# Performance work log

Measured on AMD Instinct MI355X. Metric: run time of the kernel, lower is better.

Reference implementation:

```python
import jax, jax.numpy as jnp
import numpy as np

B, T, HID = 2, 2048, 2048
H, D, QC = 16, 128, 512
RD, THETA = 64, 10000.0
WIN = 512
G, INTER = 4, 2048
EPS = 1e-6


def _rope_cache(t):
    inv = 1.0 / (THETA ** (jnp.arange(0, RD, 2, dtype=jnp.float32) / RD))  # (RD/2,)
    ang = jnp.arange(t, dtype=jnp.float32)[:, None] * inv[None, :]          # (t, RD/2)
    return jnp.cos(ang), jnp.sin(ang)


def _apply_partial_rope(x, cos, sin):
    # x: (..., t, D); rotate first RD channels (rotate-half convention)
    x_rot, x_pass = x[..., :RD], x[..., RD:]
    x1, x2 = x_rot[..., : RD // 2], x_rot[..., RD // 2 :]
    r1 = x1 * cos - x2 * sin
    r2 = x1 * sin + x2 * cos
    return jnp.concatenate([r1, r2, x_pass], axis=-1)


def _rmsnorm(x, w):
    return x * jax.lax.rsqrt(jnp.mean(x * x, axis=-1, keepdims=True) + EPS) * w


def setup_inputs() -> dict:
    key = jax.random.key(0)
    ks = jax.random.split(key, 10)
    s = 0.02
    return {
        "h": jax.random.normal(ks[0], (B, T, HID), jnp.float32),
        "wq_comp": jax.random.normal(ks[1], (HID, QC), jnp.float32) * s,
        "wq_up": jax.random.normal(ks[2], (QC, H * D), jnp.float32) * s,
        "wk": jax.random.normal(ks[3], (HID, D), jnp.float32) * s,
        "wv": jax.random.normal(ks[4], (HID, D), jnp.float32) * s,
        "q_norm_w": jnp.ones((D,), jnp.float32),
        "k_norm_w": jnp.ones((D,), jnp.float32),
        "sink_logit": jnp.zeros((H,), jnp.float32),
        "out_w1": jax.random.normal(ks[5], (G, (H // G) * D, INTER), jnp.float32) * s,
        "out_w2": jax.random.normal(ks[6], (G * INTER, HID), jnp.float32) * s,
    }


def reference(h, wq_comp, wq_up, wk, wv, q_norm_w, k_norm_w, sink_logit, out_w1, out_w2):
    b, t, _ = h.shape
    cos, sin = _rope_cache(t)
    # queries: compress -> up -> (b,H,t,D)
    q = (h @ wq_comp) @ wq_up
    q = q.reshape(b, t, H, D).transpose(0, 2, 1, 3)
    q = _rmsnorm(_apply_partial_rope(q, cos, sin), q_norm_w)
    # single shared K/V head (b,t,D)
    k = _rmsnorm(_apply_partial_rope(h @ wk, cos, sin), k_norm_w)
    v = h @ wv
    i = jnp.arange(t)
    diff = i[:, None] - i[None, :]
    mask = (diff >= 0) & (diff < WIN)  # (t,t)
    # scores (b,H,t,t) + sink column
    scale = 1.0 / jnp.sqrt(jnp.asarray(D, h.dtype))
    scores = jnp.einsum("bhtd,bsd->bhts", q, k) * scale
    scores = jnp.where(mask[None, None], scores, jnp.asarray(-1e30, h.dtype))
    sink = jnp.broadcast_to(sink_logit[None, :, None, None], (b, H, t, 1))
    probs = jax.nn.softmax(jnp.concatenate([scores, sink], axis=-1), axis=-1)
    attn = jnp.einsum("bhts,bsd->bhtd", probs[..., :t], v)  # sink mass dropped
    # grouped output projection
    x = attn.transpose(0, 2, 1, 3).reshape(b, t, G, (H // G) * D)
    x = jnp.einsum("btgi,gio->btgo", x, out_w1).reshape(b, t, G * INTER)
    return x @ out_w2
```

## Files before the change

### kernel.cpp

```cpp
#include <hip/hip_runtime.h>
#include <hip/hip_bf16.h>
#include <stdint.h>

typedef __hip_bfloat16 bf16;
typedef __bf16 bf16x8 __attribute__((ext_vector_type(8)));
typedef float f32x4 __attribute__((ext_vector_type(4)));

#define B_ 2
#define T_ 2048
#define HID_ 2048
#define H_ 16
#define D_ 128
#define WIN_ 512

__device__ __forceinline__ void async_copy16(const void* g, void* l) {
  __builtin_amdgcn_global_load_lds(
      (__attribute__((address_space(1))) void*)(uintptr_t)g,
      (__attribute__((address_space(3))) void*)(uint32_t)(uintptr_t)l,
      16, 0, 0);
}

__device__ __forceinline__ void block_sync() {
  asm volatile("" ::: "memory");
  __builtin_amdgcn_s_barrier();
  asm volatile("" ::: "memory");
}

__global__ __launch_bounds__(256) void cvt4_all(
    const float* __restrict__ h, const float* __restrict__ w1, bf16* __restrict__ outh, bf16* __restrict__ outw1)
{
  int i = blockIdx.x * 256 + threadIdx.x;
  const int NH = 2097152;
  const float* in; bf16* out;
  if (i < NH) { in = h; out = outh; }
  else { i -= NH; in = w1; out = outw1; }
  const float4 v = ((const float4*)in)[i];
  bf16* p = out + (size_t)i * 4;
  p[0] = __float2bfloat16(v.x);
  p[1] = __float2bfloat16(v.y);
  p[2] = __float2bfloat16(v.z);
  p[3] = __float2bfloat16(v.w);
}

__global__ __launch_bounds__(256) void cvtT_all(
    const float* __restrict__ wqc, const float* __restrict__ wk, const float* __restrict__ wv,
    const float* __restrict__ wqu, bf16* __restrict__ qkvT, bf16* __restrict__ wquT)
{
  __shared__ bf16 tile[32][33];
  const int id = blockIdx.x;
  const float* in; bf16* out; int R, C, bx, by;
  if (id < 1024)      { int l = id;        in = wqc; out = qkvT;                      R = 2048; C = 512;  bx = (l & 15) * 32; by = (l >> 4) * 32; }
  else if (id < 1280) { int l = id - 1024; in = wk;  out = qkvT + (size_t)512 * 2048; R = 2048; C = 128;  bx = (l & 3) * 32;  by = (l >> 2) * 32; }
  else if (id < 1536) { int l = id - 1280; in = wv;  out = qkvT + (size_t)640 * 2048; R = 2048; C = 128;  bx = (l & 3) * 32;  by = (l >> 2) * 32; }
  else                { int l = id - 1536; in = wqu; out = wquT;                      R = 512;  C = 2048; bx = (l & 63) * 32; by = (l >> 6) * 32; }
  const int tx = threadIdx.x & 31, ty = threadIdx.x >> 5;
#pragma unroll
  for (int i = 0; i < 32; i += 8)
    tile[ty+i][tx] = __float2bfloat16(in[(size_t)(by + ty + i)*C + bx + tx]);
  __syncthreads();
#pragma unroll
  for (int i = 0; i < 32; i += 8)
    out[(size_t)(bx + ty + i)*R + by + tx] = tile[tx][ty+i];
}

__global__ __launch_bounds__(256) void cvtT(
    const float* __restrict__ in, bf16* __restrict__ out, int R, int C)
{
  __shared__ bf16 tile[32][33];
  const int bx = blockIdx.x*32, by = blockIdx.y*32;
  const int tx = threadIdx.x & 31, ty = threadIdx.x >> 5;
#pragma unroll
  for (int i = 0; i < 32; i += 8)
    tile[ty+i][tx] = __float2bfloat16(in[(size_t)(by + ty + i)*C + bx + tx]);
  __syncthreads();
#pragma unroll
  for (int i = 0; i < 32; i += 8)
    out[(size_t)(bx + ty + i)*R + by + tx] = tile[tx][ty+i];
}

__global__ __launch_bounds__(256) void transpose_k(
    const bf16* __restrict__ in, bf16* __restrict__ out,
    int R, int C, int ldin, int ldout, long long inBatch, long long outBatch)
{
  __shared__ bf16 tile[32][33];
  in  += (size_t)blockIdx.z * inBatch;
  out += (size_t)blockIdx.z * outBatch;
  const int bx = blockIdx.x*32, by = blockIdx.y*32;
  const int tx = threadIdx.x & 31, ty = threadIdx.x >> 5;
#pragma unroll
  for (int i = 0; i < 32; i += 8)
    tile[ty+i][tx] = in[(size_t)(by + ty + i)*ldin + bx + tx];
  __syncthreads();
#pragma unroll
  for (int i = 0; i < 32; i += 8)
    out[(size_t)(bx + ty + i)*ldout + by + tx] = tile[tx][ty+i];
}

template <bool F32OUT>
__global__ __launch_bounds__(256) void gemm_bt(
    const bf16* __restrict__ Ab, const bf16* __restrict__ Bb, void* __restrict__ Cb,
    int K, int lda, int ldb, int ldc,
    long long sAz, long long sBz, long long sCz)
{
  const bf16* A = Ab + (size_t)blockIdx.z * sAz;
  const bf16* B = Bb + (size_t)blockIdx.z * sBz;
  __shared__ __align__(16) __bf16 sa[128*64];
  __shared__ __align__(16) __bf16 sb[128*64];
  const int bm = blockIdx.x * 128, bn = blockIdx.y * 128;
  const int t = threadIdx.x;
  const int wave = t >> 6, lane = t & 63;
  const int fm = lane & 15, quad = lane >> 4;
  const int wm = (wave & 1) * 64, wn = (wave >> 1) * 64;
  const int arow0 = t >> 3;
  const int acol_sw = (((t & 7) ^ (arow0 & 7)) << 3);
  const int fsw = fm & 7;

  f32x4 acc[4][4];
#pragma unroll
  for (int i = 0; i < 4; ++i)
#pragma unroll
    for (int j = 0; j < 4; ++j) acc[i][j] = {0.f, 0.f, 0.f, 0.f};

  for (int k0 = 0; k0 < K; k0 += 64) {
    __syncthreads();
#pragma unroll
    for (int i = 0; i < 4; ++i)
      async_copy16(&A[(size_t)(bm + arow0 + i*32)*lda + k0 + acol_sw], &sa[(size_t)(i*256 + wave*64)*8]);
#pragma unroll
    for (int i = 0; i < 4; ++i)
      async_copy16(&B[(size_t)(bn + arow0 + i*32)*ldb + k0 + acol_sw], &sb[(size_t)(i*256 + wave*64)*8]);
    __syncthreads();
#pragma unroll
    for (int ks = 0; ks < 64; ks += 32) {
      bf16x8 av[4], bv[4];
#pragma unroll
      for (int mt = 0; mt < 4; ++mt)
        av[mt] = *(const bf16x8*)&sa[(wm + mt*16 + fm)*64 + ((((ks>>3) + quad) ^ fsw) << 3)];
#pragma unroll
      for (int nt = 0; nt < 4; ++nt)
        bv[nt] = *(const bf16x8*)&sb[(wn + nt*16 + fm)*64 + ((((ks>>3) + quad) ^ fsw) << 3)];
#pragma unroll
      for (int mt = 0; mt < 4; ++mt)
#pragma unroll
        for (int nt = 0; nt < 4; ++nt)
          acc[mt][nt] = __builtin_amdgcn_mfma_f32_16x16x32_bf16(av[mt], bv[nt], acc[mt][nt], 0, 0, 0);
    }
  }
  if constexpr (F32OUT) {
    float* C = (float*)Cb + (size_t)blockIdx.z * sCz;
#pragma unroll
    for (int mt = 0; mt < 4; ++mt)
#pragma unroll
      for (int r = 0; r < 4; ++r) {
        const int row = bm + wm + mt*16 + quad*4 + r;
#pragma unroll
        for (int nt = 0; nt < 4; ++nt)
          C[(size_t)row*ldc + bn + wn + nt*16 + fm] = acc[mt][nt][r];
      }
  } else {
    bf16* C = (bf16*)Cb + (size_t)blockIdx.z * sCz;
#pragma unroll
    for (int mt = 0; mt < 4; ++mt)
#pragma unroll
      for (int r = 0; r < 4; ++r) {
        const int row = bm + wm + mt*16 + quad*4 + r;
#pragma unroll
        for (int nt = 0; nt < 4; ++nt)
          C[(size_t)row*ldc + bn + wn + nt*16 + fm] = __float2bfloat16(acc[mt][nt][r]);
      }
  }
}

template <bool F32OUT>
__global__ __launch_bounds__(512, 2) void gemm_bt8(
    const bf16* __restrict__ Ab, const bf16* __restrict__ Bb, void* __restrict__ Cb,
    int K, int lda, int ldb, int ldc,
    long long sAz, long long sBz, long long sCz)
{
  const bf16* A = Ab + (size_t)blockIdx.z * sAz;
  const bf16* B = Bb + (size_t)blockIdx.z * sBz;
  __shared__ __align__(16) __bf16 sA[2][256*64];
  __shared__ __align__(16) __bf16 sB[2][128*64];
  const int bm = blockIdx.x * 256, bn = blockIdx.y * 128;
  const int t = threadIdx.x;
  const int wave = t >> 6, lane = t & 63;
  const int fm = lane & 15, quad = lane >> 4, fsw = fm & 7;
  const int wave_m = wave >> 1, wave_n = wave & 1;
  const int srow = t >> 3;
  const int cchunk = (t & 7) ^ (srow & 7);
  const int NT = K >> 6;

  auto stage = [&](int tile, int o) {
    if (tile >= NT) return;
    const int par = tile & 1;
    const int kc = (tile << 6) + (cchunk << 3);
    if (o < 2) {
      async_copy16(&B[(size_t)(bn + (o << 6) + srow)*ldb + kc],
                   &sB[par][(size_t)((o << 6) + wave*8) * 64]);
    } else {
      const int h = (o - 2) << 7;
      async_copy16(&A[(size_t)(bm + h + srow)*lda + kc],
                   &sA[par][(size_t)(h + wave*8) * 64]);
      async_copy16(&A[(size_t)(bm + h + 64 + srow)*lda + kc],
                   &sA[par][(size_t)(h + 64 + wave*8) * 64]);
    }
  };

  f32x4 acc[4][4];
#pragma unroll
  for (int i = 0; i < 4; ++i)
#pragma unroll
    for (int j = 0; j < 4; ++j) acc[i][j] = {0.f, 0.f, 0.f, 0.f};

  stage(0, 0); stage(0, 1); stage(0, 2); stage(0, 3);
  stage(1, 0); stage(1, 1);
  asm volatile("s_waitcnt vmcnt(2)" ::: "memory");
  block_sync();

  for (int d = 0; d < NT; ++d) {
    const int par = d & 1;
    bf16x8 bfr[4][2];
#pragma unroll
    for (int q = 0; q < 4; ++q) {
      const int arow = wave_m*64 + q*16 + fm;
      const bf16x8 a0 = *(const bf16x8*)&sA[par][(size_t)arow*64 + ((quad ^ fsw) << 3)];
      const bf16x8 a1 = *(const bf16x8*)&sA[par][(size_t)arow*64 + (((4 + quad) ^ fsw) << 3)];
      if (q == 0) {
#pragma unroll
        for (int n = 0; n < 4; ++n) {
          const int brow = wave_n*64 + n*16 + fm;
          bfr[n][0] = *(const bf16x8*)&sB[par][(size_t)brow*64 + ((quad ^ fsw) << 3)];
          bfr[n][1] = *(const bf16x8*)&sB[par][(size_t)brow*64 + (((4 + quad) ^ fsw) << 3)];
        }
      }
      if (q == 0)      stage(d + 1, 2);
      else if (q == 1) stage(d + 1, 3);
      else if (q == 2) stage(d + 2, 0);
      else             stage(d + 2, 1);
      block_sync();
      __builtin_amdgcn_s_setprio(1);
#pragma unroll
      for (int n = 0; n < 4; ++n)
        acc[q][n] = __builtin_amdgcn_mfma_f32_16x16x32_bf16(a0, bfr[n][0], acc[q][n], 0, 0, 0);
#pragma unroll
      for (int n = 0; n < 4; ++n)
        acc[q][n] = __builtin_amdgcn_mfma_f32_16x16x32_bf16(a1, bfr[n][1], acc[q][n], 0, 0, 0);
      __builtin_amdgcn_s_setprio(0);
      if (q == 3 && d < NT - 1) {
        if (d == NT - 2) asm volatile("s_waitcnt vmcnt(0)" ::: "memory");
        else             asm volatile("s_waitcnt vmcnt(2)" ::: "memory");
      }
      block_sync();
    }
  }

  if constexpr (F32OUT) {
    float* C = (float*)Cb + (size_t)blockIdx.z * sCz;
#pragma unroll
    for (int q = 0; q < 4; ++q)
#pragma unroll
      for (int r = 0; r < 4; ++r) {
        const int row = bm + wave_m*64 + q*16 + quad*4 + r;
#pragma unroll
        for (int n = 0; n < 4; ++n)
          C[(size_t)row*ldc + bn + wave_n*64 + n*16 + fm] = acc[q][n][r];
      }
  } else {
    bf16* C = (bf16*)Cb + (size_t)blockIdx.z * sCz;
#pragma unroll
    for (int q = 0; q < 4; ++q)
#pragma unroll
      for (int r = 0; r < 4; ++r) {
        const int row = bm + wave_m*64 + q*16 + quad*4 + r;
#pragma unroll
        for (int n = 0; n < 4; ++n)
          C[(size_t)row*ldc + bn + wave_n*64 + n*16 + fm] = __float2bfloat16(acc[q][n][r]);
      }
  }
}

__global__ __launch_bounds__(256) void rope_rms_all(
    const bf16* __restrict__ qin, bf16* __restrict__ qout, const float* __restrict__ qw,
    const bf16* __restrict__ kin, bf16* __restrict__ kout, const float* __restrict__ kw)
{
  int blk = blockIdx.x;
  const bf16* in; bf16* out; const float* w; int in_stride, t_shift; float oscale;
  if (blk < 16384) { in = qin; out = qout; w = qw; in_stride = 128; t_shift = 4; oscale = 0.12751744f; }
  else { blk -= 16384; in = kin; out = kout; w = kw; in_stride = 768; t_shift = 0; oscale = 1.0f; }
  const int rid = blk*4 + (threadIdx.x >> 6);
  const int lane = threadIdx.x & 63;
  const bf16* row = in + (size_t)rid * in_stride;
  float e0 = __bfloat162float(row[lane]);
  float e1 = __bfloat162float(row[lane + 64]);
  float s2 = e0*e0 + e1*e1;
#pragma unroll
  for (int off = 32; off; off >>= 1) s2 += __shfl_xor(s2, off);
  const float rms = rsqrtf(s2 * (1.f/128.f) + 1e-6f) * oscale;
  const int tpos = (rid >> t_shift) & (T_ - 1);
  const int i = lane & 31;
  const float inv = expf(-(float)i * 0.28782313662425574f);
  const float ang = (float)tpos * inv;
  float sn, c;
  sincosf(ang, &sn, &c);
  const float other = __shfl_xor(e0, 32);
  const float r0 = (lane < 32) ? (e0*c - other*sn) : (other*sn + e0*c);
  bf16* orow = out + (size_t)rid * 128;
  orow[lane]      = __float2bfloat16(r0 * rms * w[lane]);
  orow[lane + 64] = __float2bfloat16(e1 * rms * w[lane + 64]);
}

__global__ __launch_bounds__(256, 3) void attn_kernel(
    const bf16* __restrict__ q,
    const bf16* __restrict__ k,
    const bf16* __restrict__ vt,
    const float* __restrict__ sink,
    bf16* __restrict__ o)
{
  __shared__ __align__(16) __bf16 sQ[64*128];
  __shared__ __align__(16) __bf16 sK[64*128];
  __shared__ __align__(16) __bf16 sV[128*64];
  const int qt = blockIdx.x, h = blockIdx.y, b = blockIdx.z;
  const int qb = qt * 64;
  const int t = threadIdx.x, wave = t >> 6, lane = t & 63;
  const int fm = lane & 15, quad = lane >> 4;
  const int fsw = fm & 7;
  const int qw = qb + wave*16;

#pragma unroll
  for (int i = 0; i < 4; ++i) {
    int chunk = i*256 + t;
    int r = chunk >> 4, c8 = (chunk & 15) ^ (r & 7);
    async_copy16(&q[(size_t)((b*T_ + qb + r)*H_ + h)*D_ + c8*8], &sQ[(size_t)(i*256 + wave*64)*8]);
  }

  bf16x8 kreg[4], vreg[4];
  auto load_kv = [&](int kb) {
#pragma unroll
    for (int i = 0; i < 4; ++i) {
      int chunk = i*256 + t;
      int r = chunk >> 4, c8 = (chunk & 15) ^ (r & 7);
      kreg[i] = *(const bf16x8*)&k[(size_t)(b*T_ + kb + r)*D_ + c8*8];
    }
#pragma unroll
    for (int i = 0; i < 4; ++i) {
      int chunk = i*256 + t;
      int d = chunk >> 3, c8 = (chunk & 7) ^ (d & 7);
      vreg[i] = *(const bf16x8*)&vt[(size_t)(b*D_ + d)*T_ + kb + c8*8];
    }
  };

  float l_run[4] = {0.f, 0.f, 0.f, 0.f};
  f32x4 oacc[8];
#pragma unroll
  for (int i = 0; i < 8; ++i) oacc[i] = {0.f, 0.f, 0.f, 0.f};

  int lo = qb - (WIN_ - 1); if (lo < 0) lo = 0;
  const int kt0 = lo >> 6;
  load_kv(kt0 * 64);

  for (int kt = kt0; kt <= qt; ++kt) {
    const int kb = kt * 64;
#pragma unroll
    for (int i = 0; i < 4; ++i)
      *(bf16x8*)&sK[(size_t)(i*256 + t)*8] = kreg[i];
#pragma unroll
    for (int i = 0; i < 4; ++i)
      *(bf16x8*)&sV[(size_t)(i*256 + t)*8] = vreg[i];
    asm volatile("s_waitcnt lgkmcnt(0)" ::: "memory");
    block_sync();
    if (kt < qt) load_kv(kb + 64);

    f32x4 s[4];
#pragma unroll
    for (int nt = 0; nt < 4; ++nt) s[nt] = {0.f, 0.f, 0.f, 0.f};
#pragma unroll
    for (int ds = 0; ds < 4; ++ds) {
      bf16x8 aq = *(const bf16x8*)&sQ[(wave*16 + fm)*128 + (((ds*4 + quad) ^ fsw) << 3)];
#pragma unroll
      for (int nt = 0; nt < 4; ++nt) {
        bf16x8 bk = *(const bf16x8*)&sK[(nt*16 + fm)*128 + (((ds*4 + quad) ^ fsw) << 3)];
        s[nt] = __builtin_amdgcn_mfma_f32_16x16x32_bf16(aq, bk, s[nt], 0, 0, 0);
      }
    }
    block_sync();

    const bool interior = (kb + 63 <= qw) && (kb >= qw - (WIN_ - 16));
    if (!interior) {
      const int qi0 = qb + wave*16 + quad*4;
#pragma unroll
      for (int nt = 0; nt < 4; ++nt) {
        const int ki = kb + nt*16 + fm;
#pragma unroll
        for (int r = 0; r < 4; ++r) {
          const int qi = qi0 + r;
          const bool ok = (ki <= qi) && (qi - ki < WIN_);
          s[nt][r] = ok ? s[nt][r] : -1e30f;
        }
      }
    }
#pragma unroll
    for (int nt = 0; nt < 4; ++nt)
#pragma unroll
      for (int r = 0; r < 4; ++r) {
        const float p = __builtin_exp2f(s[nt][r]);
        l_run[r] += p;
        sK[(wave*16 + quad*4 + r)*72 + nt*16 + fm] = __float2bfloat16(p);
      }
    asm volatile("s_waitcnt lgkmcnt(0)" ::: "memory");
#pragma unroll
    for (int ks = 0; ks < 2; ++ks) {
      bf16x8 ap = *(const bf16x8*)&sK[(wave*16 + fm)*72 + ks*32 + quad*8];
#pragma unroll
      for (int nt = 0; nt < 8; ++nt) {
        bf16x8 bv = *(const bf16x8*)&sV[(nt*16 + fm)*64 + (((ks*4 + quad) ^ fsw) << 3)];
        oacc[nt] = __builtin_amdgcn_mfma_f32_16x16x32_bf16(ap, bv, oacc[nt], 0, 0, 0);
      }
    }
    block_sync();
  }
#pragma unroll
  for (int off = 1; off < 16; off <<= 1)
#pragma unroll
    for (int r = 0; r < 4; ++r) l_run[r] += __shfl_xor(l_run[r], off);
  const float sink_p = __builtin_exp2f(sink[h] * 1.4426950408889634f);
#pragma unroll
  for (int r = 0; r < 4; ++r) {
    const int qi = qb + wave*16 + quad*4 + r;
    const float inv_l = 1.f / (l_run[r] + sink_p);
#pragma unroll
    for (int nt = 0; nt < 8; ++nt) {
      const int d = nt*16 + fm;
      o[(size_t)(b*T_ + qi)*(H_*D_) + h*D_ + d] = __float2bfloat16(oacc[nt][r] * inv_l);
    }
  }
}

extern "C" void kernel_launch(void* const* d_in, const int* in_sizes, int n_in,
                              void* d_out, int out_size, void* d_ws, size_t ws_size,
                              hipStream_t stream) {
  (void)in_sizes; (void)n_in; (void)out_size; (void)ws_size;
  const float* h       = (const float*)d_in[0];
  const float* wq_comp = (const float*)d_in[1];
  const float* wq_up   = (const float*)d_in[2];
  const float* wk      = (const float*)d_in[3];
  const float* wv      = (const float*)d_in[4];
  const float* qnw     = (const float*)d_in[5];
  const float* knw     = (const float*)d_in[6];
  const float* sink    = (const float*)d_in[7];
  const float* w1      = (const float*)d_in[8];
  const float* w2      = (const float*)d_in[9];
  float* out = (float*)d_out;
  bf16* ws   = (bf16*)d_ws;

  const size_t M1 = 1048576;
  const size_t o_hb    = 0;
  const size_t o_qr    = 8*M1;
  const size_t o_w2T   = 0;
  const size_t o_qkv   = 16*M1;
  const size_t o_WefT  = 16*M1;
  const size_t o_krt   = 20*M1;
  const size_t o_vt    = 20*M1 + 524288;
  const size_t o_wqkvT = 21*M1;
  const size_t o_wquT  = 22*M1 + 524288;
  const size_t o_w1b   = 23*M1 + 524288;
  const size_t o_x     = 27*M1 + 524288;

  const dim3 tb(256);
  cvt4_all<<<dim3(12288), tb, 0, stream>>>(h, w1, ws+o_hb, ws+o_w1b);
  cvtT_all<<<dim3(2560), tb, 0, stream>>>(wq_comp, wk, wv, wq_up, ws+o_wqkvT, ws+o_wquT);

  gemm_bt<false><<<dim3(32, 6), tb, 0, stream>>>(ws+o_hb, ws+o_wqkvT, ws+o_qkv,
                                                 2048, 2048, 2048, 768, 0, 0, 0);
  gemm_bt8<false><<<dim3(16, 16), dim3(512), 0, stream>>>(ws+o_qkv, ws+o_wquT, ws+o_qr,
                                                          512, 768, 512, 2048, 0, 0, 0);
  rope_rms_all<<<dim3(17408), tb, 0, stream>>>(ws+o_qr, ws+o_qr, qnw,
                                               ws+o_qkv + 512, ws+o_krt, knw);
  transpose_k<<<dim3(4, 64, 2), tb, 0, stream>>>(ws+o_qkv + 640, ws+o_vt, 2048, 128, 768, 2048,
                                                 (long long)2048*768, (long long)128*2048);

  attn_kernel<<<dim3(T_/64, H_, B_), tb, 0, stream>>>(ws+o_qr, ws+o_krt, ws+o_vt, sink, ws+o_x);

  cvtT<<<dim3(64, 256), tb, 0, stream>>>(w2, ws+o_w2T, 8192, 2048);
  gemm_bt8<false><<<dim3(8, 4, 4), dim3(512), 0, stream>>>(ws+o_w2T, ws+o_w1b, ws+o_WefT,
                                                           2048, 8192, 2048, 2048,
                                                           2048, (long long)512*2048, 512);
  gemm_bt8<true><<<dim3(16, 16), dim3(512), 0, stream>>>(ws+o_x, ws+o_WefT, out,
                                                         2048, 2048, 2048, 2048, 0, 0, 0);
}
```

Baseline: 354.4 us.

## Restructure GEMM main loop into two half-steps and transpose attention score MFMA

The GEMM inner loop now runs two half-iterations per K step, each loading two A row-fragments and issuing 16 MFMAs, instead of four quarter-steps with a barrier pair each. This halves the block barriers per K tile and reorders the prologue staging. The attention kernel swaps the MFMA operands so each lane holds four consecutive key scores for one query row. That lets the probabilities be packed to bf16 with v_cvt_pk_bf16_f32 and written as 8-byte stores, and shrinks the row-sum reduction to two shuffles. Larger groups between barriers may raise register pressure, and the new per-row sum gather adds a shuffle per output row.

```diff
diff --git a/kernel.cpp b/kernel.cpp
--- a/kernel.cpp
+++ b/kernel.cpp
@@ -212,46 +212,60 @@
 #pragma unroll
     for (int j = 0; j < 4; ++j) acc[i][j] = {0.f, 0.f, 0.f, 0.f};
 
-  stage(0, 0); stage(0, 1); stage(0, 2); stage(0, 3);
+  stage(0, 2); stage(0, 3); stage(0, 0); stage(0, 1);
   stage(1, 0); stage(1, 1);
   asm volatile("s_waitcnt vmcnt(2)" ::: "memory");
   block_sync();
 
   for (int d = 0; d < NT; ++d) {
     const int par = d & 1;
-    bf16x8 bfr[4][2];
-#pragma unroll
-    for (int q = 0; q < 4; ++q) {
-      const int arow = wave_m*64 + q*16 + fm;
-      const bf16x8 a0 = *(const bf16x8*)&sA[par][(size_t)arow*64 + ((quad ^ fsw) << 3)];
-      const bf16x8 a1 = *(const bf16x8*)&sA[par][(size_t)arow*64 + (((4 + quad) ^ fsw) << 3)];
-      if (q == 0) {
-#pragma unroll
-        for (int n = 0; n < 4; ++n) {
-          const int brow = wave_n*64 + n*16 + fm;
-          bfr[n][0] = *(const bf16x8*)&sB[par][(size_t)brow*64 + ((quad ^ fsw) << 3)];
-          bfr[n][1] = *(const bf16x8*)&sB[par][(size_t)brow*64 + (((4 + quad) ^ fsw) << 3)];
-        }
-      }
-      if (q == 0)      stage(d + 1, 2);
-      else if (q == 1) stage(d + 1, 3);
-      else if (q == 2) stage(d + 2, 0);
-      else             stage(d + 2, 1);
-      block_sync();
-      __builtin_amdgcn_s_setprio(1);
-#pragma unroll
-      for (int n = 0; n < 4; ++n)
-        acc[q][n] = __builtin_amdgcn_mfma_f32_16x16x32_bf16(a0, bfr[n][0], acc[q][n], 0, 0, 0);
-#pragma unroll
-      for (int n = 0; n < 4; ++n)
-        acc[q][n] = __builtin_amdgcn_mfma_f32_16x16x32_bf16(a1, bfr[n][1], acc[q][n], 0, 0, 0);
-      __builtin_amdgcn_s_setprio(0);
-      if (q == 3 && d < NT - 1) {
-        if (d == NT - 2) asm volatile("s_waitcnt vmcnt(0)" ::: "memory");
-        else             asm volatile("s_waitcnt vmcnt(2)" ::: "memory");
-      }
-      block_sync();
-    }
+    bf16x8 bfr[4][2], a01[2][2], a23[2][2];
+#pragma unroll
+    for (int n = 0; n < 4; ++n) {
+      const int brow = wave_n*64 + n*16 + fm;
+      bfr[n][0] = *(const bf16x8*)&sB[par][(size_t)brow*64 + ((quad ^ fsw) << 3)];
+      bfr[n][1] = *(const bf16x8*)&sB[par][(size_t)brow*64 + (((4 + quad) ^ fsw) << 3)];
+    }
+#pragma unroll
+    for (int qq = 0; qq < 2; ++qq) {
+      const int arow = wave_m*64 + qq*16 + fm;
+      a01[qq][0] = *(const bf16x8*)&sA[par][(size_t)arow*64 + ((quad ^ fsw) << 3)];
+      a01[qq][1] = *(const bf16x8*)&sA[par][(size_t)arow*64 + (((4 + quad) ^ fsw) << 3)];
+    }
+    stage(d + 1, 2); stage(d + 1, 3);
+    block_sync();
+    __builtin_amdgcn_s_setprio(1);
+#pragma unroll
+    for (int qq = 0; qq < 2; ++qq)
+#pragma unroll
+      for (int n = 0; n < 4; ++n) {
+        acc[qq][n] = __builtin_amdgcn_mfma_f32_16x16x32_bf16(a01[qq][0], bfr[n][0], acc[qq][n], 0, 0, 0);
+        acc[qq][n] = __builtin_amdgcn_mfma_f32_16x16x32_bf16(a01[qq][1], bfr[n][1], acc[qq][n], 0, 0, 0);
+      }
+    __builtin_amdgcn_s_setprio(0);
+    block_sync();
+#pragma unroll
+    for (int qq = 0; qq < 2; ++qq) {
+      const int arow = wave_m*64 + (2 + qq)*16 + fm;
+      a23[qq][0] = *(const bf16x8*)&sA[par][(size_t)arow*64 + ((quad ^ fsw) << 3)];
+      a23[qq][1] = *(const bf16x8*)&sA[par][(size_t)arow*64 + (((4 + quad) ^ fsw) << 3)];
+    }
+    stage(d + 2, 0); stage(d + 2, 1);
+    block_sync();
+    __builtin_amdgcn_s_setprio(1);
+#pragma unroll
+    for (int qq = 0; qq < 2; ++qq)
+#pragma unroll
+      for (int n = 0; n < 4; ++n) {
+        acc[2+qq][n] = __builtin_amdgcn_mfma_f32_16x16x32_bf16(a23[qq][0], bfr[n][0], acc[2+qq][n], 0, 0, 0);
+        acc[2+qq][n] = __builtin_amdgcn_mfma_f32_16x16x32_bf16(a23[qq][1], bfr[n][1], acc[2+qq][n], 0, 0, 0);
+      }
+    __builtin_amdgcn_s_setprio(0);
+    if (d < NT - 1) {
+      if (d == NT - 2) asm volatile("s_waitcnt vmcnt(0)" ::: "memory");
+      else             asm volatile("s_waitcnt vmcnt(2)" ::: "memory");
+    }
+    block_sync();
   }
 
   if constexpr (F32OUT) {
@@ -349,7 +363,7 @@
     }
   };
 
-  float l_run[4] = {0.f, 0.f, 0.f, 0.f};
+  float l_part = 0.f;
   f32x4 oacc[8];
 #pragma unroll
   for (int i = 0; i < 8; ++i) oacc[i] = {0.f, 0.f, 0.f, 0.f};
@@ -379,33 +393,38 @@
 #pragma unroll
       for (int nt = 0; nt < 4; ++nt) {
         bf16x8 bk = *(const bf16x8*)&sK[(nt*16 + fm)*128 + (((ds*4 + quad) ^ fsw) << 3)];
-        s[nt] = __builtin_amdgcn_mfma_f32_16x16x32_bf16(aq, bk, s[nt], 0, 0, 0);
+        s[nt] = __builtin_amdgcn_mfma_f32_16x16x32_bf16(bk, aq, s[nt], 0, 0, 0);
       }
     }
     block_sync();
 
     const bool interior = (kb + 63 <= qw) && (kb >= qw - (WIN_ - 16));
     if (!interior) {
-      const int qi0 = qb + wave*16 + quad*4;
-#pragma unroll
-      for (int nt = 0; nt < 4; ++nt) {
-        const int ki = kb + nt*16 + fm;
+      const int qi = qb + wave*16 + fm;
+#pragma unroll
+      for (int nt = 0; nt < 4; ++nt)
 #pragma unroll
         for (int r = 0; r < 4; ++r) {
-          const int qi = qi0 + r;
+          const int ki = kb + nt*16 + quad*4 + r;
           const bool ok = (ki <= qi) && (qi - ki < WIN_);
           s[nt][r] = ok ? s[nt][r] : -1e30f;
         }
-      }
     }
 #pragma unroll
     for (int nt = 0; nt < 4; ++nt)
 #pragma unroll
       for (int r = 0; r < 4; ++r) {
-        const float p = __builtin_exp2f(s[nt][r]);
-        l_run[r] += p;
-        sK[(wave*16 + quad*4 + r)*72 + nt*16 + fm] = __float2bfloat16(p);
-      }
+        s[nt][r] = __builtin_exp2f(s[nt][r]);
+        l_part += s[nt][r];
+      }
+#pragma unroll
+    for (int nt = 0; nt < 4; ++nt) {
+      uint32_t plo, phi;
+      asm("v_cvt_pk_bf16_f32 %0, %1, %2" : "=v"(plo) : "v"(s[nt][0]), "v"(s[nt][1]));
+      asm("v_cvt_pk_bf16_f32 %0, %1, %2" : "=v"(phi) : "v"(s[nt][2]), "v"(s[nt][3]));
+      uint2 pw; pw.x = plo; pw.y = phi;
+      *(uint2*)&sK[(wave*16 + fm)*72 + nt*16 + quad*4] = pw;
+    }
     asm volatile("s_waitcnt lgkmcnt(0)" ::: "memory");
 #pragma unroll
     for (int ks = 0; ks < 2; ++ks) {
@@ -418,15 +437,13 @@
     }
     block_sync();
   }
-#pragma unroll
-  for (int off = 1; off < 16; off <<= 1)
-#pragma unroll
-    for (int r = 0; r < 4; ++r) l_run[r] += __shfl_xor(l_run[r], off);
+  l_part += __shfl_xor(l_part, 16);
+  l_part += __shfl_xor(l_part, 32);
   const float sink_p = __builtin_exp2f(sink[h] * 1.4426950408889634f);
 #pragma unroll
   for (int r = 0; r < 4; ++r) {
     const int qi = qb + wave*16 + quad*4 + r;
-    const float inv_l = 1.f / (l_run[r] + sink_p);
+    const float inv_l = 1.f / (__shfl(l_part, quad*4 + r) + sink_p);
 #pragma unroll
     for (int nt = 0; nt < 8; ++nt) {
       const int d = nt*16 + fm;
```

Measured after the change: 350.0 us. No clear change (-1.2%).
